# Kernel optimization log

Hardware: AMD Instinct MI355X
Metric: run time of the kernel (lower is better)

The kernel has to match this reference:

```python
import jax, jax.numpy as jnp
import numpy as np

N, E, G = 250000, 2500000, 512
DIN, H, DEC = 6, 32, 16
BN_EPS = 1e-5


def setup_inputs() -> dict:
    key = jax.random.key(0)
    ks = iter(jax.random.split(key, 64))

    def nrm(shape, s=0.2):
        return s * jax.random.normal(next(ks), shape, jnp.float32)

    inp = {}
    inp["x"] = jax.random.normal(next(ks), (N, DIN), jnp.float32)
    inp["edge_index"] = jax.random.randint(next(ks), (2, E), 0, N)
    inp["batch"] = jnp.sort(jax.random.randint(next(ks), (N,), 0, G))
    dims = [(DIN, H), (H, H), (H, H)]
    for l, (din, dout) in enumerate(dims, 1):
        for d in ("f", "b"):
            inp[f"g{d}{l}_W1"] = nrm((din, dout))
            inp[f"g{d}{l}_b1"] = jnp.zeros((dout,), jnp.float32)
            inp[f"g{d}{l}_W2"] = nrm((dout, dout))
            inp[f"g{d}{l}_b2"] = jnp.zeros((dout,), jnp.float32)
        inp[f"bn{l}_g"] = jnp.ones((dout,), jnp.float32)
        inp[f"bn{l}_b"] = jnp.zeros((dout,), jnp.float32)
    inp["lb_W"] = nrm((H, DEC))
    inp["lb_b"] = jnp.zeros((DEC,), jnp.float32)
    inp["lm_W"] = nrm((DEC, 1))
    inp["lm_b"] = jnp.zeros((1,), jnp.float32)
    return inp


def _gin(x, src, dst, W1, b1, W2, b2):
    # PyG GINConv (eps=0): nn(x + sum_{j->i} x_j); messages flow src -> dst
    agg = jax.ops.segment_sum(x[src], dst, num_segments=x.shape[0])  # [N, d]
    h = x + agg
    return jnp.maximum(h @ W1 + b1, 0.0) @ W2 + b2


def _dgin(x, src, dst, pf, pb, gamma, beta):
    o1 = jax.nn.relu(_gin(x, src, dst, *pf))          # forward direction (A)
    o2 = jax.nn.relu(_gin(x, dst, src, *pb))          # reverse direction (A^T)
    o = 0.5 * (o1 + o2)
    mu = o.mean(0)
    var = o.var(0)  # biased var, as torch BatchNorm1d normalization
    return (o - mu) * jax.lax.rsqrt(var + BN_EPS) * gamma + beta


def reference(x, edge_index, batch,
              gf1_W1, gf1_b1, gf1_W2, gf1_b2, gb1_W1, gb1_b1, gb1_W2, gb1_b2, bn1_g, bn1_b,
              gf2_W1, gf2_b1, gf2_W2, gf2_b2, gb2_W1, gb2_b1, gb2_W2, gb2_b2, bn2_g, bn2_b,
              gf3_W1, gf3_b1, gf3_W2, gf3_b2, gb3_W1, gb3_b1, gb3_W2, gb3_b2, bn3_g, bn3_b,
              lb_W, lb_b, lm_W, lm_b):
    src, dst = edge_index[0], edge_index[1]
    h = _dgin(x, src, dst, (gf1_W1, gf1_b1, gf1_W2, gf1_b2), (gb1_W1, gb1_b1, gb1_W2, gb1_b2), bn1_g, bn1_b)
    h = _dgin(h, src, dst, (gf2_W1, gf2_b1, gf2_W2, gf2_b2), (gb2_W1, gb2_b1, gb2_W2, gb2_b2), bn2_g, bn2_b)
    h = _dgin(h, src, dst, (gf3_W1, gf3_b1, gf3_W2, gf3_b2), (gb3_W1, gb3_b1, gb3_W2, gb3_b2), bn3_g, bn3_b)
    # global mean pool over graphs
    sums = jax.ops.segment_sum(h, batch, num_segments=G)                     # [G, H]
    cnts = jax.ops.segment_sum(jnp.ones((h.shape[0],), h.dtype), batch, num_segments=G)
    pooled = sums / jnp.maximum(cnts, 1.0)[:, None]
    emb = jax.nn.relu(pooled @ lb_W + lb_b)   # dropout: identity (eval)
    return jax.nn.sigmoid(emb @ lm_W + lm_b)  # [G, 1]
```

## Files before the change

kernel.cpp:

```cpp
#include <hip/hip_runtime.h>
#include <math.h>

#define N_NODES 250000
#define N_EDGES 2500000
#define N_GRAPHS 512
#define BN_EPS 1e-5f
#define NT 500000
#define INV_N (1.0f / (float)N_NODES)
#define NBUCK 245
#define BSHIFT 10

__device__ __forceinline__ unsigned short f2bf(float x) {
    unsigned int u = __float_as_uint(x);
    unsigned int r = (u + 0x7FFFu + ((u >> 16) & 1u)) >> 16;
    return (unsigned short)r;
}
__device__ __forceinline__ float bf2f(unsigned short b) {
    return __uint_as_float(((unsigned int)b) << 16);
}


__global__ __launch_bounds__(256)
void k_histA(const int* __restrict__ src, const int* __restrict__ dst,
             int* __restrict__ gcnt, int E)
{
    __shared__ int hF[256], hB[256];
    int t = threadIdx.x;
    hF[t] = 0; hB[t] = 0;
    __syncthreads();
    for (int e = blockIdx.x * 256 + t; e < E; e += gridDim.x * 256) {
        atomicAdd(&hF[dst[e] >> BSHIFT], 1);
        atomicAdd(&hB[src[e] >> BSHIFT], 1);
    }
    __syncthreads();
    if (hF[t]) atomicAdd(&gcnt[t], hF[t]);
    if (hB[t]) atomicAdd(&gcnt[256 + t], hB[t]);
}

__global__ void k_scanBk(const int* __restrict__ gcnt,
                         int* __restrict__ bOffF, int* __restrict__ bOffB,
                         int* __restrict__ cursF, int* __restrict__ cursB,
                         int* __restrict__ off)
{
    __shared__ int s[512];
    int t = threadIdx.x;
    int vF = (t < NBUCK) ? gcnt[t] : 0;
    int vB = (t < NBUCK) ? gcnt[256 + t] : 0;
    s[t] = vF; s[256 + t] = vB;
    __syncthreads();
    for (int o = 1; o < 256; o <<= 1) {
        int xF = (t >= o) ? s[t - o] : 0;
        int xB = (t >= o) ? s[256 + t - o] : 0;
        __syncthreads();
        s[t] += xF; s[256 + t] += xB;
        __syncthreads();
    }
    int exF = s[t] - vF;
    int exB = s[256 + t] - vB;
    if (t < NBUCK) {
        bOffF[t] = exF; cursF[t] = exF;
        bOffB[t] = exB; cursB[t] = exB;
    }
    if (t == 0) {
        bOffF[NBUCK] = N_EDGES;
        bOffB[NBUCK] = N_EDGES;
        off[NT] = 2 * N_EDGES;
    }
}

__global__ __launch_bounds__(256)
void k_scatA(const int* __restrict__ src, const int* __restrict__ dst,
             int* __restrict__ cursF, int* __restrict__ cursB,
             unsigned int* __restrict__ payF, unsigned int* __restrict__ payB, int E)
{
    __shared__ int hF[256], hB[256];
    __shared__ int cF[256], cB[256];
    int t = threadIdx.x;
    hF[t] = 0; hB[t] = 0;
    __syncthreads();
    int e0 = blockIdx.x * 256 + t, STR = gridDim.x * 256;
    for (int e = e0; e < E; e += STR) {
        atomicAdd(&hF[dst[e] >> BSHIFT], 1);
        atomicAdd(&hB[src[e] >> BSHIFT], 1);
    }
    __syncthreads();
    int baseF = 0, baseB = 0;
    if (t < NBUCK) {
        if (hF[t]) baseF = atomicAdd(&cursF[t], hF[t]);
        if (hB[t]) baseB = atomicAdd(&cursB[t], hB[t]);
    }
    __syncthreads();
    cF[t] = baseF; cB[t] = baseB;
    __syncthreads();
    for (int e = e0; e < E; e += STR) {
        int s = src[e], d = dst[e];
        int tf = atomicAdd(&cF[d >> BSHIFT], 1);
        payF[tf] = ((unsigned int)(d & 1023) << 18) | (unsigned int)s;
        int tb = atomicAdd(&cB[s >> BSHIFT], 1);
        payB[tb] = ((unsigned int)(s & 1023) << 18) | (unsigned int)d;
    }
}

__global__ __launch_bounds__(256)
void k_bucket(const unsigned int* __restrict__ payF, const unsigned int* __restrict__ payB,
              const int* __restrict__ bOffF, const int* __restrict__ bOffB,
              int* __restrict__ eidx, int* __restrict__ off)
{
    __shared__ int cnt[1024];
    __shared__ int ps[256];
    int blk = blockIdx.x;
    int d  = (blk >= NBUCK) ? 1 : 0;
    int bb = blk - d * NBUCK;
    const unsigned int* pay = d ? payB : payF;
    const int* bOff = d ? bOffB : bOffF;
    int t = threadIdx.x;
    int lo = bOff[bb], hi = bOff[bb + 1];

    #pragma unroll
    for (int k = 0; k < 4; k++) cnt[t + 256 * k] = 0;
    __syncthreads();
    for (int e = lo + t; e < hi; e += 256)
        atomicAdd(&cnt[pay[e] >> 18], 1);
    __syncthreads();

    int b4 = 4 * t;
    int v0 = cnt[b4], v1 = cnt[b4 + 1], v2 = cnt[b4 + 2], v3 = cnt[b4 + 3];
    int tsum = v0 + v1 + v2 + v3;
    ps[t] = tsum;
    __syncthreads();
    for (int o = 1; o < 256; o <<= 1) {
        int x = (t >= o) ? ps[t - o] : 0;
        __syncthreads();
        ps[t] += x;
        __syncthreads();
    }
    int run = ps[t] - tsum;
    int l0 = run, l1 = run + v0, l2 = run + v0 + v1, l3 = run + v0 + v1 + v2;
    cnt[b4] = l0; cnt[b4 + 1] = l1; cnt[b4 + 2] = l2; cnt[b4 + 3] = l3;

    int gbase = d * N_EDGES + lo;
    int node0 = bb * 1024 + b4;
    if (node0 + 0 < N_NODES) off[d * N_NODES + node0 + 0] = gbase + l0;
    if (node0 + 1 < N_NODES) off[d * N_NODES + node0 + 1] = gbase + l1;
    if (node0 + 2 < N_NODES) off[d * N_NODES + node0 + 2] = gbase + l2;
    if (node0 + 3 < N_NODES) off[d * N_NODES + node0 + 3] = gbase + l3;
    __syncthreads();

    for (int e = lo + t; e < hi; e += 256) {
        unsigned int p = pay[e];
        int r = atomicAdd(&cnt[p >> 18], 1);
        eidx[gbase + r] = (int)(p & 0x3FFFFu);
    }
}


__global__ void pad_x(const float* __restrict__ x, float* __restrict__ xpad, int n)
{
    int i = blockIdx.x * blockDim.x + threadIdx.x;
    if (i >= n * 4) return;
    int node = i >> 2, p2 = i & 3;
    float2 v;
    v.x = (2 * p2     < 6) ? x[node * 6 + 2 * p2]     : 0.f;
    v.y = (2 * p2 + 1 < 6) ? x[node * 6 + 2 * p2 + 1] : 0.f;
    *(float2*)(xpad + node * 8 + 2 * p2) = v;
}


__global__ __launch_bounds__(256, 8)
void gather6p(const float* __restrict__ xpad, const int* __restrict__ off,
              const int* __restrict__ eidx, float* __restrict__ agg, int ngroups)
{
    int tid = threadIdx.x;
    int p2   = tid & 3;
    int slot = tid >> 2;
    for (int grp = blockIdx.x; grp < ngroups; grp += gridDim.x) {
        int node = grp * 64 + slot;
        bool nvalid = (node < N_NODES);
        int nd = nvalid ? node : 0;
        #pragma unroll
        for (int dir = 0; dir < 2; dir++) {
            int u = dir * N_NODES + nd;
            int k0 = off[u], k1 = off[u + 1];
            if (!nvalid) k1 = k0;
            float a0=0.f,a1=0.f,b0=0.f,b1=0.f,c0=0.f,c1=0.f,d0=0.f,d1=0.f;
            for (int p = k0; p < k1; p += 8) {
                #pragma unroll
                for (int q = 0; q < 8; q++) {
                    int kk = p + q;
                    bool act = (kk < k1);
                    int j = eidx[act ? kk : k0];
                    float2 v = *(const float2*)(xpad + j * 8 + 2 * p2);
                    float lo = act ? v.x : 0.f;
                    float hi = act ? v.y : 0.f;
                    if ((q & 3) == 0)      { a0 += lo; a1 += hi; }
                    else if ((q & 3) == 1) { b0 += lo; b1 += hi; }
                    else if ((q & 3) == 2) { c0 += lo; c1 += hi; }
                    else                   { d0 += lo; d1 += hi; }
                }
            }
            if (nvalid && p2 < 3) {
                float2 s;
                s.x = (a0 + b0) + (c0 + d0);
                s.y = (a1 + b1) + (c1 + d1);
                *(float2*)(agg + nd * 12 + dir * 6 + 2 * p2) = s;
            }
        }
    }
}


__global__ __launch_bounds__(256, 8)
void gather16(const unsigned short* __restrict__ xb, const int* __restrict__ off,
              const int* __restrict__ eidx, float* __restrict__ agg, int ngroups)
{
    const unsigned int* xu = (const unsigned int*)xb;
    int tid = threadIdx.x;
    int fp = tid & 15;
    int gg = tid >> 4;
    for (int grp = blockIdx.x; grp < ngroups; grp += gridDim.x) {
        int node = grp * 16 + gg;
        #pragma unroll
        for (int dir = 0; dir < 2; dir++) {
            int u = dir * N_NODES + node;
            int k0 = off[u], k1 = off[u + 1];
            float a0 = 0.f, a1 = 0.f, b0 = 0.f, b1 = 0.f;
            float c0 = 0.f, c1 = 0.f, d0 = 0.f, d1 = 0.f;
            for (int p = k0; p < k1; p += 8) {
                #pragma unroll
                for (int q = 0; q < 8; q++) {
                    int kk = p + q;
                    bool act = (kk < k1);
                    int j = eidx[act ? kk : k0];
                    unsigned int v = xu[j * 16 + fp];
                    float lo = act ? __uint_as_float(v << 16) : 0.f;
                    float hi = act ? __uint_as_float(v & 0xFFFF0000u) : 0.f;
                    if ((q & 3) == 0)      { a0 += lo; a1 += hi; }
                    else if ((q & 3) == 1) { b0 += lo; b1 += hi; }
                    else if ((q & 3) == 2) { c0 += lo; c1 += hi; }
                    else                   { d0 += lo; d1 += hi; }
                }
            }
            float2 s;
            s.x = (a0 + b0) + (c0 + d0);
            s.y = (a1 + b1) + (c1 + d1);
            *(float2*)(agg + node * 64 + dir * 32 + 2 * fp) = s;
        }
    }
}


__global__ __launch_bounds__(256, 6)
void gather16_12(const unsigned short* __restrict__ xb, const int* __restrict__ off,
                 const int* __restrict__ eidx, float* __restrict__ agg, int ngroups)
{
    const unsigned int* xu = (const unsigned int*)xb;
    int tid = threadIdx.x;
    int fp = tid & 15;
    int gg = tid >> 4;
    for (int grp = blockIdx.x; grp < ngroups; grp += gridDim.x) {
        int node = grp * 16 + gg;
        #pragma unroll
        for (int dir = 0; dir < 2; dir++) {
            int u = dir * N_NODES + node;
            int k0 = off[u], k1 = off[u + 1];
            float a0 = 0.f, a1 = 0.f, b0 = 0.f, b1 = 0.f;
            float c0 = 0.f, c1 = 0.f, d0 = 0.f, d1 = 0.f;
            for (int p = k0; p < k1; p += 12) {
                #pragma unroll
                for (int q = 0; q < 12; q++) {
                    int kk = p + q;
                    bool act = (kk < k1);
                    int j = eidx[act ? kk : k0];
                    unsigned int v = xu[j * 16 + fp];
                    float lo = act ? __uint_as_float(v << 16) : 0.f;
                    float hi = act ? __uint_as_float(v & 0xFFFF0000u) : 0.f;
                    if ((q & 3) == 0)      { a0 += lo; a1 += hi; }
                    else if ((q & 3) == 1) { b0 += lo; b1 += hi; }
                    else if ((q & 3) == 2) { c0 += lo; c1 += hi; }
                    else                   { d0 += lo; d1 += hi; }
                }
            }
            float2 s;
            s.x = (a0 + b0) + (c0 + d0);
            s.y = (a1 + b1) + (c1 + d1);
            *(float2*)(agg + node * 64 + dir * 32 + 2 * fp) = s;
        }
    }
}


template <int DIN, bool BN_IN, bool IN_BF16>
__global__ __launch_bounds__(256, 4)
void dgin_mlp2(const void* __restrict__ xin_v, const float* __restrict__ agg,
               const int* __restrict__ off,
               const float* __restrict__ in_stats,
               const float* __restrict__ in_g, const float* __restrict__ in_b,
               const float* __restrict__ W1f, const float* __restrict__ b1f,
               const float* __restrict__ W2f, const float* __restrict__ b2f,
               const float* __restrict__ W1b, const float* __restrict__ b1b,
               const float* __restrict__ W2b, const float* __restrict__ b2b,
               unsigned short* __restrict__ out, float* __restrict__ stats, int n)
{
    const float* xf = (const float*)xin_v;
    const unsigned short* xb = (const unsigned short*)xin_v;

    __shared__ __align__(16) float sW1[2][DIN * 32 + 8];
    __shared__ __align__(16) float sW2[2][32 * 32 + 8];
    __shared__ float sb1[2][32], sb2[2][32];
    __shared__ float sscale[32], sshift[32];
    __shared__ float sred[4 * 64];

    int tid = threadIdx.x;
    for (int i = tid; i < DIN * 32; i += 256) { sW1[0][i] = W1f[i]; sW1[1][i] = W1b[i]; }
    for (int i = tid; i < 32 * 32;  i += 256) { sW2[0][i] = W2f[i]; sW2[1][i] = W2b[i]; }
    if (tid < 32) {
        sb1[0][tid] = b1f[tid]; sb1[1][tid] = b1b[tid];
        sb2[0][tid] = b2f[tid]; sb2[1][tid] = b2b[tid];
        if (BN_IN) {
            float mu  = in_stats[tid] * INV_N;
            float var = in_stats[32 + tid] * INV_N - mu * mu;
            float sc  = in_g[tid] * rsqrtf(var + BN_EPS);
            sscale[tid] = sc;
            sshift[tid] = in_b[tid] - mu * sc;
        } else { sscale[tid] = 1.f; sshift[tid] = 0.f; }
    }
    __syncthreads();

    int nl  = tid >> 1;
    int dir = tid & 1;
    int n0 = blockIdx.x * 128 + nl;
    bool valid = (n0 < n);
    int node = valid ? n0 : (n - 1);

    float xr[DIN];
    if (IN_BF16) {
        const uint4* xp = (const uint4*)(xb + node * 32);
        #pragma unroll
        for (int q = 0; q < 4; q++) {
            uint4 u = xp[q];
            unsigned int w[4] = {u.x, u.y, u.z, u.w};
            #pragma unroll
            for (int k = 0; k < 4; k++) {
                xr[8*q + 2*k]     = __uint_as_float(w[k] << 16);
                xr[8*q + 2*k + 1] = __uint_as_float(w[k] & 0xFFFF0000u);
            }
        }
    } else {
        const float2* xp = (const float2*)(xf + node * DIN);
        #pragma unroll
        for (int q = 0; q < DIN / 2; q++) {
            float2 w = xp[q];
            xr[2*q+0] = w.x; xr[2*q+1] = w.y;
        }
    }

    float ag[DIN];
    if (DIN == 32) {
        const float4* ap = (const float4*)(agg + node * 64 + dir * 32);
        #pragma unroll
        for (int q = 0; q < 8; q++) {
            float4 w = ap[q];
            ag[4*q+0] = w.x; ag[4*q+1] = w.y; ag[4*q+2] = w.z; ag[4*q+3] = w.w;
        }
    } else {
        const float* ap = agg + node * (2 * DIN) + dir * DIN;
        #pragma unroll
        for (int i = 0; i < DIN; i++) ag[i] = ap[i];
    }
    int ob = dir * N_NODES + node;
    float degp1 = (float)(off[ob + 1] - off[ob] + 1);

    float t1[32];
    #pragma unroll
    for (int j = 0; j < 32; j++) t1[j] = sb1[dir][j];
    #pragma unroll
    for (int i = 0; i < DIN; i++) {
        float hv = xr[i] + ag[i];
        if (BN_IN) hv = fmaf(sscale[i], hv, degp1 * sshift[i]);
        const float4* wr = (const float4*)(&sW1[dir][i * 32]);
        #pragma unroll
        for (int q = 0; q < 8; q++) {
            float4 w = wr[q];
            t1[4*q+0] = fmaf(hv, w.x, t1[4*q+0]);
            t1[4*q+1] = fmaf(hv, w.y, t1[4*q+1]);
            t1[4*q+2] = fmaf(hv, w.z, t1[4*q+2]);
            t1[4*q+3] = fmaf(hv, w.w, t1[4*q+3]);
        }
    }
    #pragma unroll
    for (int j = 0; j < 32; j++) t1[j] = fmaxf(t1[j], 0.f);

    float o2[32];
    #pragma unroll
    for (int j = 0; j < 32; j++) o2[j] = sb2[dir][j];
    #pragma unroll
    for (int i = 0; i < 32; i++) {
        float hv = t1[i];
        const float4* wr = (const float4*)(&sW2[dir][i * 32]);
        #pragma unroll
        for (int q = 0; q < 8; q++) {
            float4 w = wr[q];
            o2[4*q+0] = fmaf(hv, w.x, o2[4*q+0]);
            o2[4*q+1] = fmaf(hv, w.y, o2[4*q+1]);
            o2[4*q+2] = fmaf(hv, w.z, o2[4*q+2]);
            o2[4*q+3] = fmaf(hv, w.w, o2[4*q+3]);
        }
    }

    float o[32];
    #pragma unroll
    for (int j = 0; j < 32; j++) {
        float r  = fmaxf(o2[j], 0.f);
        float pr = __shfl_xor(r, 1);
        o[j] = 0.5f * (r + pr);
    }

    #pragma unroll
    for (int j = 0; j < 32; j++) o[j] = bf2f(f2bf(o[j]));

    if (valid) {
        uint4* op = (uint4*)(out + node * 32);
        if (dir == 0) {
            uint4 u;
            u.x = (unsigned int)f2bf(o[0])  | ((unsigned int)f2bf(o[1])  << 16);
            u.y = (unsigned int)f2bf(o[2])  | ((unsigned int)f2bf(o[3])  << 16);
            u.z = (unsigned int)f2bf(o[4])  | ((unsigned int)f2bf(o[5])  << 16);
            u.w = (unsigned int)f2bf(o[6])  | ((unsigned int)f2bf(o[7])  << 16);
            op[0] = u;
            u.x = (unsigned int)f2bf(o[8])  | ((unsigned int)f2bf(o[9])  << 16);
            u.y = (unsigned int)f2bf(o[10]) | ((unsigned int)f2bf(o[11]) << 16);
            u.z = (unsigned int)f2bf(o[12]) | ((unsigned int)f2bf(o[13]) << 16);
            u.w = (unsigned int)f2bf(o[14]) | ((unsigned int)f2bf(o[15]) << 16);
            op[1] = u;
        } else {
            uint4 u;
            u.x = (unsigned int)f2bf(o[16]) | ((unsigned int)f2bf(o[17]) << 16);
            u.y = (unsigned int)f2bf(o[18]) | ((unsigned int)f2bf(o[19]) << 16);
            u.z = (unsigned int)f2bf(o[20]) | ((unsigned int)f2bf(o[21]) << 16);
            u.w = (unsigned int)f2bf(o[22]) | ((unsigned int)f2bf(o[23]) << 16);
            op[2] = u;
            u.x = (unsigned int)f2bf(o[24]) | ((unsigned int)f2bf(o[25]) << 16);
            u.y = (unsigned int)f2bf(o[26]) | ((unsigned int)f2bf(o[27]) << 16);
            u.z = (unsigned int)f2bf(o[28]) | ((unsigned int)f2bf(o[29]) << 16);
            u.w = (unsigned int)f2bf(o[30]) | ((unsigned int)f2bf(o[31]) << 16);
            op[3] = u;
        }
    }

    int lane = tid & 63;
    int wave = tid >> 6;
    #pragma unroll
    for (int f = 0; f < 32; f++) {
        float v = (valid && dir == 0) ? o[f] : 0.f;
        float v2 = v * v;
        #pragma unroll
        for (int offs = 32; offs > 0; offs >>= 1) {
            v  += __shfl_down(v, offs);
            v2 += __shfl_down(v2, offs);
        }
        if (lane == 0) {
            sred[wave * 64 + f]      = v;
            sred[wave * 64 + 32 + f] = v2;
        }
    }
    __syncthreads();
    if (tid < 64) {
        float a = sred[tid] + sred[64 + tid] + sred[128 + tid] + sred[192 + tid];
        atomicAdd(&stats[tid], a);
    }
}


__global__ void pool_seg(const unsigned short* __restrict__ h, const int* __restrict__ batch,
                         float* __restrict__ psum, float* __restrict__ pcnt, int n)
{
    int tid = threadIdx.x;
    int grp = tid >> 5, f = tid & 31;
    int base = blockIdx.x * 256;
    float acc = 0.f, cnt = 0.f;
    int curg = -1;
    for (int it = 0; it < 32; it++) {
        int nd = base + grp + it * 8;
        if (nd < n) {
            int g = batch[nd];
            if (g != curg) {
                if (curg >= 0) {
                    atomicAdd(&psum[curg * 32 + f], acc);
                    if (f == 0) atomicAdd(&pcnt[curg], cnt);
                }
                curg = g; acc = 0.f; cnt = 0.f;
            }
            acc += bf2f(h[nd * 32 + f]);
            cnt += 1.f;
        }
    }
    if (curg >= 0) {
        atomicAdd(&psum[curg * 32 + f], acc);
        if (f == 0) atomicAdd(&pcnt[curg], cnt);
    }
}

__global__ void head_kernel(const float* __restrict__ psum, const float* __restrict__ pcnt,
                            const float* __restrict__ stats3,
                            const float* __restrict__ g3, const float* __restrict__ b3,
                            const float* __restrict__ lbW, const float* __restrict__ lbb,
                            const float* __restrict__ lmW, const float* __restrict__ lmb,
                            float* __restrict__ out)
{
    int g = threadIdx.x;
    float cnt = fmaxf(pcnt[g], 1.0f);
    float inv = 1.0f / cnt;
    float p[32];
    #pragma unroll
    for (int i = 0; i < 32; i++) {
        float mu  = stats3[i] * INV_N;
        float var = stats3[32 + i] * INV_N - mu * mu;
        float a   = g3[i] * rsqrtf(var + BN_EPS);
        float b   = b3[i] - mu * a;
        p[i] = fmaf(a, psum[g * 32 + i] * inv, b);
    }
    float z = lmb[0];
    #pragma unroll
    for (int k = 0; k < 16; k++) {
        float acc = lbb[k];
        #pragma unroll
        for (int i = 0; i < 32; i++) acc += p[i] * lbW[i * 16 + k];
        z += fmaxf(acc, 0.0f) * lmW[k];
    }
    out[g] = 1.0f / (1.0f + expf(-z));
}


extern "C" void kernel_launch(void* const* d_in, const int* in_sizes, int n_in,
                              void* d_out, int out_size, void* d_ws, size_t ws_size,
                              hipStream_t stream)
{
    const float* x   = (const float*)d_in[0];
    const int* ei    = (const int*)d_in[1];
    const int* batch = (const int*)d_in[2];
    const int* src = ei;
    const int* dst = ei + N_EDGES;
    char* ws = (char*)d_ws;

    auto W = [&](int l, int j) { return (const float*)d_in[3 + (l - 1) * 10 + j]; };

    unsigned short* h = (unsigned short*)(ws + 0);
    float* xpad = (float*)(ws + 16000016);
    float* agg  = (float*)(ws + 32000000);
    int*   eidx = (int*)  (ws + 96000000);
    int*   off  = (int*)  (ws + 116000000);
    int* gcnt  = (int*)(ws + 32000000);
    int* bOffF = (int*)(ws + 32002048);
    int* bOffB = (int*)(ws + 32003072);
    int* cursF = (int*)(ws + 32004096);
    int* cursB = (int*)(ws + 32005120);
    unsigned int* payF = (unsigned int*)(ws + 32008192);
    unsigned int* payB = (unsigned int*)(ws + 42008192);
    float* stats1 = (float*)(ws + 118000016);
    float* stats2 = stats1 + 64;
    float* stats3 = stats1 + 128;
    float* psum   = (float*)(ws + 118000784);
    float* pcnt   = (float*)(ws + 118066320);

    hipMemsetAsync(gcnt, 0, 2048, stream);
    k_histA<<<1024, 256, 0, stream>>>(src, dst, gcnt, N_EDGES);
    k_scanBk<<<1, 256, 0, stream>>>(gcnt, bOffF, bOffB, cursF, cursB, off);
    k_scatA<<<384, 256, 0, stream>>>(src, dst, cursF, cursB, payF, payB, N_EDGES);
    k_bucket<<<2 * NBUCK, 256, 0, stream>>>(payF, payB, bOffF, bOffB, eidx, off);

    pad_x<<<(N_NODES * 4 + 255) / 256, 256, 0, stream>>>(x, xpad, N_NODES);
    hipMemsetAsync(stats1, 0, 3 * 64 * 4, stream);

    const int GG   = 4096;
    const int NG64 = (N_NODES + 63) / 64;
    const int NG16 = N_NODES / 16;
    const int GM   = (N_NODES + 127) / 128;

    gather6p<<<GG, 256, 0, stream>>>(xpad, off, eidx, agg, NG64);
    dgin_mlp2<6, false, false><<<GM, 256, 0, stream>>>(
        x, agg, off, nullptr, nullptr, nullptr,
        W(1,0), W(1,1), W(1,2), W(1,3), W(1,4), W(1,5), W(1,6), W(1,7),
        h, stats1, N_NODES);

    gather16<<<GG, 256, 0, stream>>>(h, off, eidx, agg, NG16);
    dgin_mlp2<32, true, true><<<GM, 256, 0, stream>>>(
        h, agg, off, stats1, W(1,8), W(1,9),
        W(2,0), W(2,1), W(2,2), W(2,3), W(2,4), W(2,5), W(2,6), W(2,7),
        h, stats2, N_NODES);

    gather16_12<<<GG, 256, 0, stream>>>(h, off, eidx, agg, NG16);
    dgin_mlp2<32, true, true><<<GM, 256, 0, stream>>>(
        h, agg, off, stats2, W(2,8), W(2,9),
        W(3,0), W(3,1), W(3,2), W(3,3), W(3,4), W(3,5), W(3,6), W(3,7),
        h, stats3, N_NODES);

    hipMemsetAsync(psum, 0, (size_t)N_GRAPHS * 32 * 4, stream);
    hipMemsetAsync(pcnt, 0, (size_t)N_GRAPHS * 4, stream);
    pool_seg<<<(N_NODES + 255) / 256, 256, 0, stream>>>(h, batch, psum, pcnt, N_NODES);
    head_kernel<<<1, 512, 0, stream>>>(psum, pcnt, stats3, W(3,8), W(3,9),
        (const float*)d_in[33], (const float*)d_in[34],
        (const float*)d_in[35], (const float*)d_in[36],
        (float*)d_out);
}
```

Before: 881.5 us.

## Split MLP output features across thread pair instead of splitting directions

Each thread pair previously split the two GIN directions, and each thread computed all 32 output features for its direction. Now both threads run both directions, each computing 16 of the 32 output features, and they exchange the hidden activations through shuffles for the second layer. This halves the per-thread register arrays, which should ease register pressure at the requested occupancy. It also removes the final cross-lane averaging and lets both threads share the store and the BN stat reduction. In exchange it adds 32 shuffles per direction and loads the aggregation rows for both directions in every thread.

```diff
diff --git a/kernel.cpp b/kernel.cpp
--- a/kernel.cpp
+++ b/kernel.cpp
@@ -304,8 +304,8 @@
     const float* xf = (const float*)xin_v;
     const unsigned short* xb = (const unsigned short*)xin_v;
 
-    __shared__ __align__(16) float sW1[2][DIN * 32 + 8];
-    __shared__ __align__(16) float sW2[2][32 * 32 + 8];
+    __shared__ __align__(16) float sW1[2][DIN * 32];
+    __shared__ __align__(16) float sW2[2][32 * 32];
     __shared__ float sb1[2][32], sb2[2][32];
     __shared__ float sscale[32], sshift[32];
     __shared__ float sred[4 * 64];
@@ -327,7 +327,8 @@
     __syncthreads();
 
     int nl  = tid >> 1;
-    int dir = tid & 1;
+    int par = tid & 1;
+    int fb  = 16 * par;
     int n0 = blockIdx.x * 128 + nl;
     bool valid = (n0 < n);
     int node = valid ? n0 : (n - 1);
@@ -354,113 +355,105 @@
         }
     }
 
-    float ag[DIN];
-    if (DIN == 32) {
-        const float4* ap = (const float4*)(agg + node * 64 + dir * 32);
-        #pragma unroll
-        for (int q = 0; q < 8; q++) {
-            float4 w = ap[q];
-            ag[4*q+0] = w.x; ag[4*q+1] = w.y; ag[4*q+2] = w.z; ag[4*q+3] = w.w;
-        }
-    } else {
-        const float* ap = agg + node * (2 * DIN) + dir * DIN;
-        #pragma unroll
-        for (int i = 0; i < DIN; i++) ag[i] = ap[i];
-    }
-    int ob = dir * N_NODES + node;
-    float degp1 = (float)(off[ob + 1] - off[ob] + 1);
-
-    float t1[32];
+    float o[16];
+
     #pragma unroll
-    for (int j = 0; j < 32; j++) t1[j] = sb1[dir][j];
+    for (int dir = 0; dir < 2; dir++) {
+        float ag[DIN];
+        if (DIN == 32) {
+            const float4* ap = (const float4*)(agg + node * 64 + dir * 32);
+            #pragma unroll
+            for (int q = 0; q < 8; q++) {
+                float4 w = ap[q];
+                ag[4*q+0] = w.x; ag[4*q+1] = w.y; ag[4*q+2] = w.z; ag[4*q+3] = w.w;
+            }
+        } else {
+            const float* ap = agg + node * (2 * DIN) + dir * DIN;
+            #pragma unroll
+            for (int i = 0; i < DIN; i++) ag[i] = ap[i];
+        }
+        int ob = dir * N_NODES + node;
+        float degp1 = (float)(off[ob + 1] - off[ob] + 1);
+
+        float t1[16];
+        #pragma unroll
+        for (int j = 0; j < 16; j++) t1[j] = sb1[dir][fb + j];
+        #pragma unroll
+        for (int i = 0; i < DIN; i++) {
+            float hv = xr[i] + ag[i];
+            if (BN_IN) hv = fmaf(sscale[i], hv, degp1 * sshift[i]);
+            const float4* wr = (const float4*)(&sW1[dir][i * 32 + fb]);
+            #pragma unroll
+            for (int q = 0; q < 4; q++) {
+                float4 w = wr[q];
+                t1[4*q+0] = fmaf(hv, w.x, t1[4*q+0]);
+                t1[4*q+1] = fmaf(hv, w.y, t1[4*q+1]);
+                t1[4*q+2] = fmaf(hv, w.z, t1[4*q+2]);
+                t1[4*q+3] = fmaf(hv, w.w, t1[4*q+3]);
+            }
+        }
+        #pragma unroll
+        for (int j = 0; j < 16; j++) t1[j] = fmaxf(t1[j], 0.f);
+
+        float o2[16];
+        #pragma unroll
+        for (int j = 0; j < 16; j++) o2[j] = sb2[dir][fb + j];
+        #pragma unroll
+        for (int i = 0; i < 32; i++) {
+            float own  = t1[i & 15];
+            float part = __shfl_xor(own, 1);
+            float hv = ((i >> 4) == par) ? own : part;
+            const float4* wr = (const float4*)(&sW2[dir][i * 32 + fb]);
+            #pragma unroll
+            for (int q = 0; q < 4; q++) {
+                float4 w = wr[q];
+                o2[4*q+0] = fmaf(hv, w.x, o2[4*q+0]);
+                o2[4*q+1] = fmaf(hv, w.y, o2[4*q+1]);
+                o2[4*q+2] = fmaf(hv, w.z, o2[4*q+2]);
+                o2[4*q+3] = fmaf(hv, w.w, o2[4*q+3]);
+            }
+        }
+        if (dir == 0) {
+            #pragma unroll
+            for (int j = 0; j < 16; j++) o[j] = fmaxf(o2[j], 0.f);
+        } else {
+            #pragma unroll
+            for (int j = 0; j < 16; j++) o[j] = 0.5f * (o[j] + fmaxf(o2[j], 0.f));
+        }
+    }
+
     #pragma unroll
-    for (int i = 0; i < DIN; i++) {
-        float hv = xr[i] + ag[i];
-        if (BN_IN) hv = fmaf(sscale[i], hv, degp1 * sshift[i]);
-        const float4* wr = (const float4*)(&sW1[dir][i * 32]);
-        #pragma unroll
-        for (int q = 0; q < 8; q++) {
-            float4 w = wr[q];
-            t1[4*q+0] = fmaf(hv, w.x, t1[4*q+0]);
-            t1[4*q+1] = fmaf(hv, w.y, t1[4*q+1]);
-            t1[4*q+2] = fmaf(hv, w.z, t1[4*q+2]);
-            t1[4*q+3] = fmaf(hv, w.w, t1[4*q+3]);
-        }
-    }
-    #pragma unroll
-    for (int j = 0; j < 32; j++) t1[j] = fmaxf(t1[j], 0.f);
-
-    float o2[32];
-    #pragma unroll
-    for (int j = 0; j < 32; j++) o2[j] = sb2[dir][j];
-    #pragma unroll
-    for (int i = 0; i < 32; i++) {
-        float hv = t1[i];
-        const float4* wr = (const float4*)(&sW2[dir][i * 32]);
-        #pragma unroll
-        for (int q = 0; q < 8; q++) {
-            float4 w = wr[q];
-            o2[4*q+0] = fmaf(hv, w.x, o2[4*q+0]);
-            o2[4*q+1] = fmaf(hv, w.y, o2[4*q+1]);
-            o2[4*q+2] = fmaf(hv, w.z, o2[4*q+2]);
-            o2[4*q+3] = fmaf(hv, w.w, o2[4*q+3]);
-        }
-    }
-
-    float o[32];
-    #pragma unroll
-    for (int j = 0; j < 32; j++) {
-        float r  = fmaxf(o2[j], 0.f);
-        float pr = __shfl_xor(r, 1);
-        o[j] = 0.5f * (r + pr);
-    }
-
-    #pragma unroll
-    for (int j = 0; j < 32; j++) o[j] = bf2f(f2bf(o[j]));
+    for (int j = 0; j < 16; j++) o[j] = bf2f(f2bf(o[j]));
 
     if (valid) {
-        uint4* op = (uint4*)(out + node * 32);
-        if (dir == 0) {
-            uint4 u;
-            u.x = (unsigned int)f2bf(o[0])  | ((unsigned int)f2bf(o[1])  << 16);
-            u.y = (unsigned int)f2bf(o[2])  | ((unsigned int)f2bf(o[3])  << 16);
-            u.z = (unsigned int)f2bf(o[4])  | ((unsigned int)f2bf(o[5])  << 16);
-            u.w = (unsigned int)f2bf(o[6])  | ((unsigned int)f2bf(o[7])  << 16);
-            op[0] = u;
-            u.x = (unsigned int)f2bf(o[8])  | ((unsigned int)f2bf(o[9])  << 16);
-            u.y = (unsigned int)f2bf(o[10]) | ((unsigned int)f2bf(o[11]) << 16);
-            u.z = (unsigned int)f2bf(o[12]) | ((unsigned int)f2bf(o[13]) << 16);
-            u.w = (unsigned int)f2bf(o[14]) | ((unsigned int)f2bf(o[15]) << 16);
-            op[1] = u;
-        } else {
-            uint4 u;
-            u.x = (unsigned int)f2bf(o[16]) | ((unsigned int)f2bf(o[17]) << 16);
-            u.y = (unsigned int)f2bf(o[18]) | ((unsigned int)f2bf(o[19]) << 16);
-            u.z = (unsigned int)f2bf(o[20]) | ((unsigned int)f2bf(o[21]) << 16);
-            u.w = (unsigned int)f2bf(o[22]) | ((unsigned int)f2bf(o[23]) << 16);
-            op[2] = u;
-            u.x = (unsigned int)f2bf(o[24]) | ((unsigned int)f2bf(o[25]) << 16);
-            u.y = (unsigned int)f2bf(o[26]) | ((unsigned int)f2bf(o[27]) << 16);
-            u.z = (unsigned int)f2bf(o[28]) | ((unsigned int)f2bf(o[29]) << 16);
-            u.w = (unsigned int)f2bf(o[30]) | ((unsigned int)f2bf(o[31]) << 16);
-            op[3] = u;
-        }
+        uint4* op = (uint4*)(out + node * 32) + 2 * par;
+        uint4 u;
+        u.x = (unsigned int)f2bf(o[0])  | ((unsigned int)f2bf(o[1])  << 16);
+        u.y = (unsigned int)f2bf(o[2])  | ((unsigned int)f2bf(o[3])  << 16);
+        u.z = (unsigned int)f2bf(o[4])  | ((unsigned int)f2bf(o[5])  << 16);
+        u.w = (unsigned int)f2bf(o[6])  | ((unsigned int)f2bf(o[7])  << 16);
+        op[0] = u;
+        u.x = (unsigned int)f2bf(o[8])  | ((unsigned int)f2bf(o[9])  << 16);
+        u.y = (unsigned int)f2bf(o[10]) | ((unsigned int)f2bf(o[11]) << 16);
+        u.z = (unsigned int)f2bf(o[12]) | ((unsigned int)f2bf(o[13]) << 16);
+        u.w = (unsigned int)f2bf(o[14]) | ((unsigned int)f2bf(o[15]) << 16);
+        op[1] = u;
     }
 
     int lane = tid & 63;
     int wave = tid >> 6;
     #pragma unroll
-    for (int f = 0; f < 32; f++) {
-        float v = (valid && dir == 0) ? o[f] : 0.f;
+    for (int j = 0; j < 16; j++) {
+        float v = valid ? o[j] : 0.f;
         float v2 = v * v;
         #pragma unroll
-        for (int offs = 32; offs > 0; offs >>= 1) {
+        for (int offs = 32; offs >= 2; offs >>= 1) {
             v  += __shfl_down(v, offs);
             v2 += __shfl_down(v2, offs);
         }
-        if (lane == 0) {
-            sred[wave * 64 + f]      = v;
-            sred[wave * 64 + 32 + f] = v2;
+        if (lane < 2) {
+            sred[wave * 64 + fb + j]      = v;
+            sred[wave * 64 + 32 + fb + j] = v2;
         }
     }
     __syncthreads();
```

Measured after the change: 825.7 us. 1.07x faster.
